# Kernel optimization log

Hardware: AMD Instinct MI355X
Metric: run time of the kernel (lower is better)

The kernel has to match this reference:

```python
import jax, jax.numpy as jnp
import numpy as np

B, N, D = 256, 2048, 128
ANCHOR = 0


def setup_inputs() -> dict:
    key = jax.random.key(0)
    k0, k1, k2, k3 = jax.random.split(key, 4)
    return {
        "embs": jax.random.normal(k0, (B * N, D), jnp.float32),
        "W1": jax.random.normal(k1, (D, 2 * D), jnp.float32) / np.sqrt(2 * D),
        "b1": jnp.zeros((D,), jnp.float32),
        "W2": jax.random.normal(k2, (D, D), jnp.float32) / np.sqrt(D),
        "b2": jnp.zeros((D,), jnp.float32),
        "batch_idx": jax.random.randint(k3, (B * N,), 0, B, dtype=jnp.int32),
        "batch_size": B,
        "num_nodes": N,
        "num_anchors": ANCHOR,
    }


def reference(embs, W1, b1, W2, b2, batch_idx, batch_size, num_nodes, num_anchors):
    # static boolean mask over nodes (num_anchors is a Python int)
    non_target = np.arange(num_nodes) != num_anchors
    e = embs.reshape(batch_size, num_nodes, -1)            # (B, N, D)
    non_targets = e[:, non_target]                          # (B, N-1, D)
    target = e[:, ~non_target]                              # (B, 1, D)
    x = jnp.concatenate(
        (jnp.broadcast_to(target, non_targets.shape), non_targets), axis=-1
    )                                                       # (B, N-1, 2D)
    h = jax.nn.relu(jnp.einsum("bnk,dk->bnd", x, W1) + b1)  # (B, N-1, D)
    y = jnp.einsum("bnk,dk->bnd", h, W2) + b2               # (B, N-1, D)
    y = y.reshape(batch_size * (num_nodes - 1), -1)
    bidx = batch_idx.reshape(batch_size, num_nodes)[:, non_target].reshape(-1)
    return jax.ops.segment_sum(y, bidx, num_segments=batch_size)  # (B, D)
```

## Files before the change

### kernel.cpp

```cpp
#include <hip/hip_runtime.h>

#define B_SZ    256
#define N_NODES 2048
#define D_DIM   128
#define NROW_TOT (B_SZ * N_NODES)

typedef __attribute__((ext_vector_type(8))) short short8;
typedef __attribute__((ext_vector_type(4))) float f32x4;

#define WS_W1BF   0
#define WS_COUNT  65536
#define WS_T      66560
#define WS_ACC    197632
#define WS_P      459776
#define CAP       4096
#define WS_NEEDED (WS_P + B_SZ * CAP * 4)

__device__ __forceinline__ unsigned pk2(float x, float y) {
    unsigned a = __float_as_uint(x), b = __float_as_uint(y);
    a += 0x7fffu + ((a >> 16) & 1u);
    b += 0x7fffu + ((b >> 16) & 1u);
    return (a >> 16) | (b & 0xffff0000u);
}

__global__ void k_prep(const float* __restrict__ W1, unsigned* __restrict__ w1bf,
                       const int* __restrict__ bidx, int* __restrict__ count,
                       int* __restrict__ P, const float* __restrict__ embs,
                       const float* __restrict__ b1, float* __restrict__ T) {
    int t = threadIdx.x;
    if (blockIdx.x < 64) {
        int i = blockIdx.x * 256 + t;
        float2 f = ((const float2*)W1)[i];
        w1bf[i] = pk2(f.x, f.y);
        return;
    }
    if (blockIdx.x >= 576) {
        int tb = blockIdx.x - 576;
        __shared__ float trow[128];
        if (t < 128) trow[t] = embs[(size_t)(tb << 11) * D_DIM + t];
        __syncthreads();
        if (t < 128) {
            const float4* w = (const float4*)(W1 + t * 256);
            float s = 0.f;
#pragma unroll
            for (int k = 0; k < 32; k++) {
                float4 wv = w[k];
                s += trow[4 * k + 0] * wv.x + trow[4 * k + 1] * wv.y
                   + trow[4 * k + 2] * wv.z + trow[4 * k + 3] * wv.w;
            }
            T[tb * 128 + t] = s + b1[t];
        }
        return;
    }
    __shared__ int lh[256];
    __shared__ int sbase[256];
    int blk = blockIdx.x - 64;
    lh[t] = 0;
    __syncthreads();
    int base = blk * 1024 + t * 4;
    int4 v = ((const int4*)bidx)[blk * 256 + t];
    int p0 = -1, p1 = -1, p2 = -1, p3 = -1;
    if (((base + 0) & 2047) != 0) p0 = atomicAdd(&lh[v.x], 1);
    if (((base + 1) & 2047) != 0) p1 = atomicAdd(&lh[v.y], 1);
    if (((base + 2) & 2047) != 0) p2 = atomicAdd(&lh[v.z], 1);
    if (((base + 3) & 2047) != 0) p3 = atomicAdd(&lh[v.w], 1);
    __syncthreads();
    if (lh[t]) sbase[t] = atomicAdd(&count[t], lh[t]);
    __syncthreads();
    if (p0 >= 0) P[v.x * CAP + sbase[v.x] + p0] = base + 0;
    if (p1 >= 0) P[v.y * CAP + sbase[v.y] + p1] = base + 1;
    if (p2 >= 0) P[v.z * CAP + sbase[v.z] + p2] = base + 2;
    if (p3 >= 0) P[v.w * CAP + sbase[v.w] + p3] = base + 3;
}

#define CHUNK   64
#define ESTRIDE 272

__global__ __launch_bounds__(512, 4) void k_main(
    const float* __restrict__ embs, const float* __restrict__ Tm,
    const short* __restrict__ w1bf, const int* __restrict__ P,
    const int* __restrict__ count, float* __restrict__ ACC)
{
    __shared__ __align__(16) char estage[2][CHUNK * ESTRIDE];
    __shared__ int   bidarr[2][64];
    __shared__ float segacc[D_DIM];

    int tid  = threadIdx.x;
    int g    = blockIdx.x;
    int s    = g >> 1;
    int half = g & 1;
    int cnt  = count[s];
    const int pbase = s * CAP;

    if (tid < D_DIM) segacc[tid] = 0.f;

    int lane = tid & 63;
    int wid  = tid >> 6;
    int rt   = wid & 1;
    int cg   = wid >> 1;
    int q    = lane >> 4;
    int i15  = lane & 15;

    short8 bfrag[4][2];
#pragma unroll
    for (int kt = 0; kt < 4; kt++)
#pragma unroll
        for (int ct = 0; ct < 2; ct++) {
            int n = cg * 32 + ct * 16 + i15;
            bfrag[kt][ct] = *(const short8*)(w1bf + n * 256 + 128 + kt * 32 + q * 8);
        }

    int srow = tid >> 3;
    int part = tid & 7;

    int nct = (cnt + CHUNK - 1) >> 6;
    int myn = (nct > half) ? ((nct - half + 1) >> 1) : 0;

    float4 f0, f1, f2, f3;
    int bcur = 0, ridx_next = 0;

    if (myn > 0) {
        int rl = half * 64 + srow;
        int r0 = P[pbase + (rl < cnt ? rl : cnt - 1)];
        bcur = r0 >> 11;
        const float4* src = (const float4*)(embs + (size_t)r0 * D_DIM) + part * 4;
        f0 = src[0]; f1 = src[1]; f2 = src[2]; f3 = src[3];
        if (myn > 1) {
            int rl2 = (half + 2) * 64 + srow;
            ridx_next = P[pbase + (rl2 < cnt ? rl2 : cnt - 1)];
        }
    }
    __syncthreads();

    float asum0 = 0.f, asum1 = 0.f;

    for (int i = 0; i < myn; i++) {
        int c = half + 2 * i;
        char* wb = estage[i & 1];
        {
            uint4 wa = make_uint4(pk2(f0.x, f0.y), pk2(f0.z, f0.w),
                                  pk2(f1.x, f1.y), pk2(f1.z, f1.w));
            uint4 wv = make_uint4(pk2(f2.x, f2.y), pk2(f2.z, f2.w),
                                  pk2(f3.x, f3.y), pk2(f3.z, f3.w));
            uint4* dst = (uint4*)(wb + srow * ESTRIDE + part * 32);
            dst[0] = wa; dst[1] = wv;
            if (part == 0) bidarr[i & 1][srow] = bcur;
        }
        __syncthreads();

        int4 bh0 = *(const int4*)&bidarr[i & 1][rt * 32 + q * 4];
        int4 bh1 = *(const int4*)&bidarr[i & 1][rt * 32 + 16 + q * 4];
        int c0 = cg * 32 + i15;
        float tv0[4][2], tv1[4][2];
#pragma unroll
        for (int j = 0; j < 4; j++) {
            int b0 = (&bh0.x)[j], b1i = (&bh1.x)[j];
            tv0[j][0] = Tm[b0 * 128 + c0];  tv0[j][1] = Tm[b0 * 128 + c0 + 16];
            tv1[j][0] = Tm[b1i * 128 + c0]; tv1[j][1] = Tm[b1i * 128 + c0 + 16];
        }

        if (i + 1 < myn) {
            int r = ridx_next;
            bcur = r >> 11;
            const float4* src = (const float4*)(embs + (size_t)r * D_DIM) + part * 4;
            f0 = src[0]; f1 = src[1]; f2 = src[2]; f3 = src[3];
            if (i + 2 < myn) {
                int rl = (c + 4) * 64 + srow;
                ridx_next = P[pbase + (rl < cnt ? rl : cnt - 1)];
            }
        }

        f32x4 m00 = {0,0,0,0}, m01 = {0,0,0,0}, m10 = {0,0,0,0}, m11 = {0,0,0,0};
        const char* ar0 = wb + (rt * 32 + i15) * ESTRIDE + q * 16;
        const char* ar1 = ar0 + 16 * ESTRIDE;
#pragma unroll
        for (int kt = 0; kt < 4; kt++) {
            short8 a0 = *(const short8*)(ar0 + kt * 64);
            short8 a1 = *(const short8*)(ar1 + kt * 64);
            m00 = __builtin_amdgcn_mfma_f32_16x16x32_bf16(a0, bfrag[kt][0], m00, 0, 0, 0);
            m01 = __builtin_amdgcn_mfma_f32_16x16x32_bf16(a0, bfrag[kt][1], m01, 0, 0, 0);
            m10 = __builtin_amdgcn_mfma_f32_16x16x32_bf16(a1, bfrag[kt][0], m10, 0, 0, 0);
            m11 = __builtin_amdgcn_mfma_f32_16x16x32_bf16(a1, bfrag[kt][1], m11, 0, 0, 0);
        }
        int rb0 = c * 64 + rt * 32 + q * 4;
        int rb1 = rb0 + 16;
#pragma unroll
        for (int j = 0; j < 4; j++) {
            if (rb0 + j < cnt) {
                asum0 += fmaxf(m00[j] + tv0[j][0], 0.f);
                asum1 += fmaxf(m01[j] + tv0[j][1], 0.f);
            }
            if (rb1 + j < cnt) {
                asum0 += fmaxf(m10[j] + tv1[j][0], 0.f);
                asum1 += fmaxf(m11[j] + tv1[j][1], 0.f);
            }
        }
    }

    asum0 += __shfl_xor(asum0, 16, 64);
    asum0 += __shfl_xor(asum0, 32, 64);
    asum1 += __shfl_xor(asum1, 16, 64);
    asum1 += __shfl_xor(asum1, 32, 64);
    if (lane < 16) {
        atomicAdd(&segacc[cg * 32 + lane],      asum0);
        atomicAdd(&segacc[cg * 32 + 16 + lane], asum1);
    }
    __syncthreads();
    if (tid < D_DIM) ACC[g * D_DIM + tid] = segacc[tid];
}

__global__ void k_out(const float* __restrict__ ACC, const float* __restrict__ W2,
                      const float* __restrict__ b2, const int* __restrict__ count,
                      float* __restrict__ out) {
    __shared__ float a[D_DIM];
    int s = blockIdx.x, d = threadIdx.x;
    a[d] = ACC[(2 * s) * D_DIM + d] + ACC[(2 * s + 1) * D_DIM + d];
    __syncthreads();
    float sum = (float)count[s] * b2[d];
    const float4* w = (const float4*)(W2 + d * D_DIM);
#pragma unroll
    for (int k = 0; k < 32; k++) {
        float4 wv = w[k];
        sum += a[4 * k + 0] * wv.x + a[4 * k + 1] * wv.y
             + a[4 * k + 2] * wv.z + a[4 * k + 3] * wv.w;
    }
    out[s * D_DIM + d] = sum;
}

extern "C" void kernel_launch(void* const* d_in, const int* in_sizes, int n_in,
                              void* d_out, int out_size, void* d_ws, size_t ws_size,
                              hipStream_t stream) {
    const float* embs = (const float*)d_in[0];
    const float* W1   = (const float*)d_in[1];
    const float* b1   = (const float*)d_in[2];
    const float* W2   = (const float*)d_in[3];
    const float* b2   = (const float*)d_in[4];
    const int*   bidx = (const int*)d_in[5];

    char* ws = (char*)d_ws;
    unsigned* w1bf_u = (unsigned*)(ws + WS_W1BF);
    short*    w1bf   = (short*)(ws + WS_W1BF);
    int*   count  = (int*)(ws + WS_COUNT);
    float* T      = (float*)(ws + WS_T);
    float* ACC    = (float*)(ws + WS_ACC);
    int*   P      = (int*)(ws + WS_P);

    hipMemsetAsync(count, 0, 256 * sizeof(int), stream);
    k_prep<<<832, 256, 0, stream>>>(W1, w1bf_u, bidx, count, P, embs, b1, T);
    k_main<<<512, 512, 0, stream>>>(embs, T, w1bf, P, count, ACC);
    k_out<<<256, 128, 0, stream>>>(ACC, W2, b2, count, (float*)d_out);
}
```

Before: 403.4 us.

## Stream embeddings contiguously and accumulate per-segment sums in LDS bins

Removes the bucketing pass that built per-segment row index lists and the gathered row loads in the main kernel. Each block now streams a contiguous slice of rows, runs the bf16 MFMA, and scatters ReLU outputs into a full 256x128 shared-memory bin array using LDS atomics with a rotation to spread bank conflicts. Each block writes its partial bins to global memory, and the output kernel reduces 256 partials per segment before applying W2. The cost is about 128KB of LDS per block, so only one block fits per CU. It also adds heavy LDS atomic traffic and about 32MB of extra partial-sum writes and reads.

```diff
diff --git a/kernel.cpp b/kernel.cpp
--- a/kernel.cpp
+++ b/kernel.cpp
@@ -7,14 +7,13 @@
 
 typedef __attribute__((ext_vector_type(8))) short short8;
 typedef __attribute__((ext_vector_type(4))) float f32x4;
+typedef __attribute__((ext_vector_type(4))) unsigned uint4v;
 
 #define WS_W1BF   0
 #define WS_COUNT  65536
 #define WS_T      66560
 #define WS_ACC    197632
-#define WS_P      459776
-#define CAP       4096
-#define WS_NEEDED (WS_P + B_SZ * CAP * 4)
+#define WS_NEEDED (WS_ACC + 256 * B_SZ * D_DIM * 4)
 
 __device__ __forceinline__ unsigned pk2(float x, float y) {
     unsigned a = __float_as_uint(x), b = __float_as_uint(y);
@@ -24,9 +23,8 @@
 }
 
 __global__ void k_prep(const float* __restrict__ W1, unsigned* __restrict__ w1bf,
-                       const int* __restrict__ bidx, int* __restrict__ count,
-                       int* __restrict__ P, const float* __restrict__ embs,
-                       const float* __restrict__ b1, float* __restrict__ T) {
+                       const float* __restrict__ embs, const float* __restrict__ b1,
+                       float* __restrict__ T) {
     int t = threadIdx.x;
     if (blockIdx.x < 64) {
         int i = blockIdx.x * 256 + t;
@@ -34,179 +32,123 @@
         w1bf[i] = pk2(f.x, f.y);
         return;
     }
-    if (blockIdx.x >= 576) {
-        int tb = blockIdx.x - 576;
-        __shared__ float trow[128];
-        if (t < 128) trow[t] = embs[(size_t)(tb << 11) * D_DIM + t];
-        __syncthreads();
-        if (t < 128) {
-            const float4* w = (const float4*)(W1 + t * 256);
-            float s = 0.f;
-#pragma unroll
-            for (int k = 0; k < 32; k++) {
-                float4 wv = w[k];
-                s += trow[4 * k + 0] * wv.x + trow[4 * k + 1] * wv.y
-                   + trow[4 * k + 2] * wv.z + trow[4 * k + 3] * wv.w;
-            }
-            T[tb * 128 + t] = s + b1[t];
-        }
-        return;
-    }
-    __shared__ int lh[256];
-    __shared__ int sbase[256];
-    int blk = blockIdx.x - 64;
-    lh[t] = 0;
-    __syncthreads();
-    int base = blk * 1024 + t * 4;
-    int4 v = ((const int4*)bidx)[blk * 256 + t];
-    int p0 = -1, p1 = -1, p2 = -1, p3 = -1;
-    if (((base + 0) & 2047) != 0) p0 = atomicAdd(&lh[v.x], 1);
-    if (((base + 1) & 2047) != 0) p1 = atomicAdd(&lh[v.y], 1);
-    if (((base + 2) & 2047) != 0) p2 = atomicAdd(&lh[v.z], 1);
-    if (((base + 3) & 2047) != 0) p3 = atomicAdd(&lh[v.w], 1);
-    __syncthreads();
-    if (lh[t]) sbase[t] = atomicAdd(&count[t], lh[t]);
-    __syncthreads();
-    if (p0 >= 0) P[v.x * CAP + sbase[v.x] + p0] = base + 0;
-    if (p1 >= 0) P[v.y * CAP + sbase[v.y] + p1] = base + 1;
-    if (p2 >= 0) P[v.z * CAP + sbase[v.z] + p2] = base + 2;
-    if (p3 >= 0) P[v.w * CAP + sbase[v.w] + p3] = base + 3;
-}
-
-#define CHUNK   64
-#define ESTRIDE 272
-
-__global__ __launch_bounds__(512, 4) void k_main(
+    int tb = blockIdx.x - 64;
+    __shared__ float trow[128];
+    if (t < 128) trow[t] = embs[(size_t)(tb << 11) * D_DIM + t];
+    __syncthreads();
+    if (t < 128) {
+        const float4* w = (const float4*)(W1 + t * 256);
+        float s = 0.f;
+#pragma unroll
+        for (int k = 0; k < 32; k++) {
+            float4 wv = w[k];
+            s += trow[4 * k + 0] * wv.x + trow[4 * k + 1] * wv.y
+               + trow[4 * k + 2] * wv.z + trow[4 * k + 3] * wv.w;
+        }
+        T[tb * 128 + t] = s + b1[t];
+    }
+}
+
+__global__ __launch_bounds__(512, 2) void k_main(
     const float* __restrict__ embs, const float* __restrict__ Tm,
-    const short* __restrict__ w1bf, const int* __restrict__ P,
-    const int* __restrict__ count, float* __restrict__ ACC)
+    const short* __restrict__ w1bf, const int* __restrict__ bidx,
+    int* __restrict__ count, float* __restrict__ ACC)
 {
-    __shared__ __align__(16) char estage[2][CHUNK * ESTRIDE];
-    __shared__ int   bidarr[2][64];
-    __shared__ float segacc[D_DIM];
-
-    int tid  = threadIdx.x;
-    int g    = blockIdx.x;
-    int s    = g >> 1;
-    int half = g & 1;
-    int cnt  = count[s];
-    const int pbase = s * CAP;
-
-    if (tid < D_DIM) segacc[tid] = 0.f;
+    __shared__ float bins[B_SZ * D_DIM];
+    __shared__ int   cbin[B_SZ];
+
+    int tid = threadIdx.x;
+#pragma unroll
+    for (int i = 0; i < 16; i++)
+        ((float4*)bins)[tid + i * 512] = make_float4(0.f, 0.f, 0.f, 0.f);
+    if (tid < B_SZ) cbin[tid] = 0;
 
     int lane = tid & 63;
     int wid  = tid >> 6;
-    int rt   = wid & 1;
-    int cg   = wid >> 1;
     int q    = lane >> 4;
     int i15  = lane & 15;
 
-    short8 bfrag[4][2];
+    short8 bfrag[4][8];
 #pragma unroll
     for (int kt = 0; kt < 4; kt++)
 #pragma unroll
-        for (int ct = 0; ct < 2; ct++) {
-            int n = cg * 32 + ct * 16 + i15;
-            bfrag[kt][ct] = *(const short8*)(w1bf + n * 256 + 128 + kt * 32 + q * 8);
-        }
-
-    int srow = tid >> 3;
-    int part = tid & 7;
-
-    int nct = (cnt + CHUNK - 1) >> 6;
-    int myn = (nct > half) ? ((nct - half + 1) >> 1) : 0;
-
-    float4 f0, f1, f2, f3;
-    int bcur = 0, ridx_next = 0;
-
-    if (myn > 0) {
-        int rl = half * 64 + srow;
-        int r0 = P[pbase + (rl < cnt ? rl : cnt - 1)];
-        bcur = r0 >> 11;
-        const float4* src = (const float4*)(embs + (size_t)r0 * D_DIM) + part * 4;
-        f0 = src[0]; f1 = src[1]; f2 = src[2]; f3 = src[3];
-        if (myn > 1) {
-            int rl2 = (half + 2) * 64 + srow;
-            ridx_next = P[pbase + (rl2 < cnt ? rl2 : cnt - 1)];
-        }
-    }
-    __syncthreads();
-
-    float asum0 = 0.f, asum1 = 0.f;
-
-    for (int i = 0; i < myn; i++) {
-        int c = half + 2 * i;
-        char* wb = estage[i & 1];
-        {
-            uint4 wa = make_uint4(pk2(f0.x, f0.y), pk2(f0.z, f0.w),
-                                  pk2(f1.x, f1.y), pk2(f1.z, f1.w));
-            uint4 wv = make_uint4(pk2(f2.x, f2.y), pk2(f2.z, f2.w),
-                                  pk2(f3.x, f3.y), pk2(f3.z, f3.w));
-            uint4* dst = (uint4*)(wb + srow * ESTRIDE + part * 32);
-            dst[0] = wa; dst[1] = wv;
-            if (part == 0) bidarr[i & 1][srow] = bcur;
-        }
-        __syncthreads();
-
-        int4 bh0 = *(const int4*)&bidarr[i & 1][rt * 32 + q * 4];
-        int4 bh1 = *(const int4*)&bidarr[i & 1][rt * 32 + 16 + q * 4];
-        int c0 = cg * 32 + i15;
-        float tv0[4][2], tv1[4][2];
+        for (int nt = 0; nt < 8; nt++)
+            bfrag[kt][nt] = *(const short8*)(w1bf + (nt * 16 + i15) * 256 + 128 + kt * 32 + q * 8);
+
+    int wstart = (blockIdx.x * 8 + wid) * 256;
+    int tb = wstart >> 11;
+    float tv[8];
+#pragma unroll
+    for (int nt = 0; nt < 8; nt++) tv[nt] = Tm[tb * 128 + nt * 16 + i15];
+
+    __syncthreads();
+
+    const float* base = embs + (size_t)(wstart + i15) * D_DIM + q * 8;
+
+    float4 raw[8];
+#pragma unroll
+    for (int kt = 0; kt < 4; kt++) {
+        raw[2 * kt]     = *(const float4*)(base + kt * 32);
+        raw[2 * kt + 1] = *(const float4*)(base + kt * 32 + 4);
+    }
+
+    for (int t = 0; t < 16; t++) {
+        short8 a[4];
+#pragma unroll
+        for (int kt = 0; kt < 4; kt++) {
+            union { uint4v u; short8 s; } cv;
+            float4 lo = raw[2 * kt], hi = raw[2 * kt + 1];
+            cv.u = (uint4v){pk2(lo.x, lo.y), pk2(lo.z, lo.w),
+                            pk2(hi.x, hi.y), pk2(hi.z, hi.w)};
+            a[kt] = cv.s;
+        }
+        int tilebase = wstart + t * 16;
+        int4 sg = *(const int4*)(bidx + tilebase + q * 4);
+
+        if (t < 15) {
+            const float* nb = base + (t + 1) * (16 * D_DIM);
+#pragma unroll
+            for (int kt = 0; kt < 4; kt++) {
+                raw[2 * kt]     = *(const float4*)(nb + kt * 32);
+                raw[2 * kt + 1] = *(const float4*)(nb + kt * 32 + 4);
+            }
+        }
+
+        f32x4 acc[8] = {{0,0,0,0},{0,0,0,0},{0,0,0,0},{0,0,0,0},
+                        {0,0,0,0},{0,0,0,0},{0,0,0,0},{0,0,0,0}};
+#pragma unroll
+        for (int kt = 0; kt < 4; kt++)
+#pragma unroll
+            for (int nt = 0; nt < 8; nt++)
+                acc[nt] = __builtin_amdgcn_mfma_f32_16x16x32_bf16(a[kt], bfrag[kt][nt], acc[nt], 0, 0, 0);
+
 #pragma unroll
         for (int j = 0; j < 4; j++) {
-            int b0 = (&bh0.x)[j], b1i = (&bh1.x)[j];
-            tv0[j][0] = Tm[b0 * 128 + c0];  tv0[j][1] = Tm[b0 * 128 + c0 + 16];
-            tv1[j][0] = Tm[b1i * 128 + c0]; tv1[j][1] = Tm[b1i * 128 + c0 + 16];
-        }
-
-        if (i + 1 < myn) {
-            int r = ridx_next;
-            bcur = r >> 11;
-            const float4* src = (const float4*)(embs + (size_t)r * D_DIM) + part * 4;
-            f0 = src[0]; f1 = src[1]; f2 = src[2]; f3 = src[3];
-            if (i + 2 < myn) {
-                int rl = (c + 4) * 64 + srow;
-                ridx_next = P[pbase + (rl < cnt ? rl : cnt - 1)];
+            int row = tilebase + q * 4 + j;
+            int seg = (&sg.x)[j];
+            if ((row & 2047) != 0) {
+                if (i15 == 0) atomicAdd(&cbin[seg], 1);
+                int rot = (seg << 2);
+#pragma unroll
+                for (int nt = 0; nt < 8; nt++) {
+                    float v = fmaxf(acc[nt][j] + tv[nt], 0.f);
+                    atomicAdd(&bins[seg * 128 + ((nt * 16 + i15 + rot) & 127)], v);
+                }
             }
         }
-
-        f32x4 m00 = {0,0,0,0}, m01 = {0,0,0,0}, m10 = {0,0,0,0}, m11 = {0,0,0,0};
-        const char* ar0 = wb + (rt * 32 + i15) * ESTRIDE + q * 16;
-        const char* ar1 = ar0 + 16 * ESTRIDE;
-#pragma unroll
-        for (int kt = 0; kt < 4; kt++) {
-            short8 a0 = *(const short8*)(ar0 + kt * 64);
-            short8 a1 = *(const short8*)(ar1 + kt * 64);
-            m00 = __builtin_amdgcn_mfma_f32_16x16x32_bf16(a0, bfrag[kt][0], m00, 0, 0, 0);
-            m01 = __builtin_amdgcn_mfma_f32_16x16x32_bf16(a0, bfrag[kt][1], m01, 0, 0, 0);
-            m10 = __builtin_amdgcn_mfma_f32_16x16x32_bf16(a1, bfrag[kt][0], m10, 0, 0, 0);
-            m11 = __builtin_amdgcn_mfma_f32_16x16x32_bf16(a1, bfrag[kt][1], m11, 0, 0, 0);
-        }
-        int rb0 = c * 64 + rt * 32 + q * 4;
-        int rb1 = rb0 + 16;
-#pragma unroll
-        for (int j = 0; j < 4; j++) {
-            if (rb0 + j < cnt) {
-                asum0 += fmaxf(m00[j] + tv0[j][0], 0.f);
-                asum1 += fmaxf(m01[j] + tv0[j][1], 0.f);
-            }
-            if (rb1 + j < cnt) {
-                asum0 += fmaxf(m10[j] + tv1[j][0], 0.f);
-                asum1 += fmaxf(m11[j] + tv1[j][1], 0.f);
-            }
-        }
-    }
-
-    asum0 += __shfl_xor(asum0, 16, 64);
-    asum0 += __shfl_xor(asum0, 32, 64);
-    asum1 += __shfl_xor(asum1, 16, 64);
-    asum1 += __shfl_xor(asum1, 32, 64);
-    if (lane < 16) {
-        atomicAdd(&segacc[cg * 32 + lane],      asum0);
-        atomicAdd(&segacc[cg * 32 + 16 + lane], asum1);
-    }
-    __syncthreads();
-    if (tid < D_DIM) ACC[g * D_DIM + tid] = segacc[tid];
+    }
+
+    __syncthreads();
+    if (tid < B_SZ && cbin[tid]) atomicAdd(&count[tid], cbin[tid]);
+    float* accout = ACC + (size_t)blockIdx.x * (B_SZ * D_DIM);
+#pragma unroll
+    for (int i = 0; i < 16; i++) {
+        int idx = tid + i * 512;
+        int s   = idx >> 5;
+        int d4  = (idx & 31) << 2;
+        float4 v = *(const float4*)&bins[s * 128 + ((d4 + (s << 2)) & 127)];
+        *(float4*)(accout + s * 128 + d4) = v;
+    }
 }
 
 __global__ void k_out(const float* __restrict__ ACC, const float* __restrict__ W2,
@@ -214,7 +156,16 @@
                       float* __restrict__ out) {
     __shared__ float a[D_DIM];
     int s = blockIdx.x, d = threadIdx.x;
-    a[d] = ACC[(2 * s) * D_DIM + d] + ACC[(2 * s + 1) * D_DIM + d];
+    const float* p = ACC + s * D_DIM + d;
+    float s0 = 0.f, s1 = 0.f, s2 = 0.f, s3 = 0.f;
+#pragma unroll 4
+    for (int b = 0; b < 256; b += 4) {
+        s0 += p[(size_t)(b + 0) * (B_SZ * D_DIM)];
+        s1 += p[(size_t)(b + 1) * (B_SZ * D_DIM)];
+        s2 += p[(size_t)(b + 2) * (B_SZ * D_DIM)];
+        s3 += p[(size_t)(b + 3) * (B_SZ * D_DIM)];
+    }
+    a[d] = (s0 + s1) + (s2 + s3);
     __syncthreads();
     float sum = (float)count[s] * b2[d];
     const float4* w = (const float4*)(W2 + d * D_DIM);
@@ -243,10 +194,9 @@
     int*   count  = (int*)(ws + WS_COUNT);
     float* T      = (float*)(ws + WS_T);
     float* ACC    = (float*)(ws + WS_ACC);
-    int*   P      = (int*)(ws + WS_P);
-
-    hipMemsetAsync(count, 0, 256 * sizeof(int), stream);
-    k_prep<<<832, 256, 0, stream>>>(W1, w1bf_u, bidx, count, P, embs, b1, T);
-    k_main<<<512, 512, 0, stream>>>(embs, T, w1bf, P, count, ACC);
+
+    hipMemsetAsync(count, 0, B_SZ * sizeof(int), stream);
+    k_prep<<<320, 256, 0, stream>>>(W1, w1bf_u, embs, b1, T);
+    k_main<<<256, 512, 0, stream>>>(embs, T, w1bf, bidx, count, ACC);
     k_out<<<256, 128, 0, stream>>>(ACC, W2, b2, count, (float*)d_out);
 }
```

Result: slower. 651.7 us (+61.5%).
